# Kernel tuning notes

Hardware: AMD Instinct MI355X
Metric: run time of the kernel (lower is better)

Reference implementation:

```python
import jax, jax.numpy as jnp
import numpy as np

N, E, D, T = 10000, 320000, 128, 128


def _layer_norm(x, g, b, eps=1e-5):
    mu = jnp.mean(x, axis=-1, keepdims=True)
    var = jnp.mean(jnp.square(x - mu), axis=-1, keepdims=True)
    return (x - mu) * jax.lax.rsqrt(var + eps) * g + b


def setup_inputs() -> dict:
    key = jax.random.key(0)
    ks = jax.random.split(key, 24)
    s = 0.05

    def lin(k, fin, fout):
        k1, k2 = jax.random.split(k)
        return (jax.random.normal(k1, (fin, fout), jnp.float32) * s,
                jax.random.normal(k2, (fout,), jnp.float32) * s)

    W_tp, b_tp = lin(ks[5], T, D)
    W_sg, b_sg = lin(ks[6], D, D)
    W_dg, b_dg = lin(ks[7], D, D)
    W_eg, b_eg = lin(ks[8], D, D)
    W_su, b_su = lin(ks[9], D, D)
    W_du, b_du = lin(ks[10], D, D)
    return {
        'node_feats': jax.random.normal(ks[0], (N, D), jnp.float32),
        'edge_feats': jax.random.normal(ks[1], (E, D), jnp.float32),
        'time_feats': jax.random.normal(ks[2], (N, T), jnp.float32),
        'src': jax.random.randint(ks[3], (E,), 0, N),
        'dst': jax.random.randint(ks[4], (E,), 0, N),
        'W_tp': W_tp, 'b_tp': b_tp,
        'W_sg': W_sg, 'b_sg': b_sg,
        'W_dg': W_dg, 'b_dg': b_dg,
        'W_eg': W_eg, 'b_eg': b_eg,
        'W_su': W_su, 'b_su': b_su,
        'W_du': W_du, 'b_du': b_du,
        'ln_e_g': jnp.ones((D,), jnp.float32), 'ln_e_b': jnp.zeros((D,), jnp.float32),
        'ln_n_g': jnp.ones((D,), jnp.float32), 'ln_n_b': jnp.zeros((D,), jnp.float32),
    }


def reference(node_feats, edge_feats, time_feats, src, dst,
              W_tp, b_tp, W_sg, b_sg, W_dg, b_dg, W_eg, b_eg,
              W_su, b_su, W_du, b_du, ln_e_g, ln_e_b, ln_n_g, ln_n_b):
    n_nodes = node_feats.shape[0]
    # per-node gate projections (time proj folded into source gate)
    e_src = node_feats @ W_sg + b_sg + time_feats @ W_tp + b_tp   # [N, D]
    e_dst = node_feats @ W_dg + b_dg                              # [N, D]
    # edge gating: gather from both endpoints + edge feature projection
    m = e_src[src] + e_dst[dst] + edge_feats @ W_eg + b_eg        # [E, D]
    sigma = jax.nn.sigmoid(m)                                     # [E, D]
    # gated message passing: scatter-add over destination nodes
    Bh = node_feats @ W_du + b_du                                 # [N, D]
    sum_sigma_h = jax.ops.segment_sum(Bh[src] * sigma, dst, num_segments=n_nodes)
    sum_sigma = jax.ops.segment_sum(sigma, dst, num_segments=n_nodes)
    h = sum_sigma_h / (sum_sigma + 1e-6)                          # [N, D]
    x = node_feats @ W_su + b_su + h
    x = jax.nn.silu(_layer_norm(x, ln_n_g, ln_n_b))
    y = jax.nn.silu(_layer_norm(m, ln_e_g, ln_e_b))
    x = node_feats + x  # residual
    y = edge_feats + y
    return (x, y)
```

## Files before the change

kernel.cpp:

```cpp
#include <hip/hip_runtime.h>
#include <hip/hip_bf16.h>

#define N_NODES 10000
#define N_EDGES 320000
#define D 128
#define NBINS 10000

typedef float f32x4 __attribute__((ext_vector_type(4)));
typedef float f32x2 __attribute__((ext_vector_type(2)));
typedef short bf16x8 __attribute__((ext_vector_type(8)));
typedef short bf16x16 __attribute__((ext_vector_type(16)));

static __device__ inline short f2bf(float f) {
    union { __hip_bfloat16 h; short s; } u;
    u.h = __float2bfloat16(f);
    return u.s;
}

static __device__ inline float bf2f(short s) {
    union { float f; unsigned u; } x;
    x.u = ((unsigned)(unsigned short)s) << 16;
    return x.f;
}

static __device__ inline float fast_rcp(float x) { return __builtin_amdgcn_rcpf(x); }

__global__ void prep_hist(const float* __restrict__ W_sg, const float* __restrict__ W_tp,
                          const float* __restrict__ W_dg, const float* __restrict__ W_du,
                          const float* __restrict__ W_su, const float* __restrict__ W_eg,
                          short* __restrict__ Wsrc, short* __restrict__ Wdg,
                          short* __restrict__ Wdu, short* __restrict__ Wsu,
                          short* __restrict__ Weg,
                          const int* __restrict__ dst, int* __restrict__ cnt) {
    int bid = blockIdx.x;
    if (bid < 1250) {
        int i = bid * 256 + threadIdx.x;
        atomicAdd(&cnt[dst[i]], 1);
        return;
    }
    int idx = (bid - 1250) * 256 + threadIdx.x;
    const float* W0; const float* W1; short* out; int i2;
    if (idx < 32768)      { W0 = W_sg; W1 = W_tp; out = Wsrc; i2 = idx; }
    else if (idx < 49152) { W0 = W_dg; W1 = W_dg; out = Wdg;  i2 = idx - 32768; }
    else if (idx < 65536) { W0 = W_du; W1 = W_du; out = Wdu;  i2 = idx - 49152; }
    else if (idx < 81920) { W0 = W_su; W1 = W_su; out = Wsu;  i2 = idx - 65536; }
    else                  { W0 = W_eg; W1 = W_eg; out = Weg;  i2 = idx - 81920; }
    int b  = i2 & 7;
    int l  = (i2 >> 3) & 63;
    int jt = (i2 >> 9) & 7;
    int t  = i2 >> 12;
    int k = 32 * t + ((l >> 4) * 8) + b;
    int j = jt * 16 + (l & 15);
    float v = (k < 128) ? W0[k * 128 + j] : W1[(k - 128) * 128 + j];
    out[i2] = f2bf(v);
}

__launch_bounds__(1024)
__global__ void scan_kernel(const int* __restrict__ cnt, int* __restrict__ cursor) {
    __shared__ int s[1024];
    int t = threadIdx.x;
    int b0 = t * 10;
    int loc[10];
    int tot = 0;
#pragma unroll
    for (int i = 0; i < 10; ++i) {
        int v = (b0 + i < NBINS) ? cnt[b0 + i] : 0;
        loc[i] = tot; tot += v;
    }
    s[t] = tot;
    __syncthreads();
    for (int off = 1; off < 1024; off <<= 1) {
        int v = (t >= off) ? s[t - off] : 0;
        __syncthreads();
        s[t] += v;
        __syncthreads();
    }
    int base = (t == 0) ? 0 : s[t - 1];
#pragma unroll
    for (int i = 0; i < 10; ++i)
        if (b0 + i < NBINS) cursor[b0 + i] = base + loc[i];
}

__global__ void scatter_kernel(const int* __restrict__ src, const int* __restrict__ dst,
                               int* __restrict__ cursor,
                               int* __restrict__ perm,
                               int* __restrict__ src_s, int* __restrict__ dst_s) {
    int i = blockIdx.x * 256 + threadIdx.x;
    if (i < N_EDGES) {
        int d = dst[i];
        int p = atomicAdd(&cursor[d], 1);
        perm[p] = i;
        src_s[p] = src[i];
        dst_s[p] = d;
    }
}

__launch_bounds__(256)
__global__ void node_proj_kernel(const float* __restrict__ node,
                                 const float* __restrict__ timef,
                                 const short* __restrict__ Wsrc_pk,
                                 const short* __restrict__ Wdg_pk,
                                 const short* __restrict__ Wdu_pk,
                                 const short* __restrict__ Wsu_pk,
                                 const float* __restrict__ b_sg, const float* __restrict__ b_tp,
                                 const float* __restrict__ b_dg, const float* __restrict__ b_du,
                                 const float* __restrict__ b_su, const float* __restrict__ b_eg,
                                 short* __restrict__ spk,
                                 short* __restrict__ dpk,
                                 float* __restrict__ xs,
                                 float* __restrict__ ss, float* __restrict__ ssh) {
    {
        int r0b = blockIdx.x * 64;
        int nrows = N_NODES - r0b; if (nrows > 64) nrows = 64;
        f32x4 z = {0.f, 0.f, 0.f, 0.f};
        f32x4* s4 = (f32x4*)(ss + (size_t)r0b * D);
        f32x4* h4 = (f32x4*)(ssh + (size_t)r0b * D);
        int nch = nrows * D / 4;
        for (int i = threadIdx.x; i < nch; i += 256) { s4[i] = z; h4[i] = z; }
    }

    int tid = threadIdx.x;
    int w = tid >> 6;
    int l = tid & 63;
    int g = l >> 4;
    int lr = l & 15;
    int r0 = blockIdx.x * 64 + w * 16;
    int arow = r0 + lr;

    bf16x8 aN[4], aT[4];
    if (arow < N_NODES) {
        const float* np = node + (size_t)arow * D;
        const float* tp = timef + (size_t)arow * D;
#pragma unroll
        for (int t = 0; t < 4; ++t) {
            int k0 = 32 * t + g * 8;
            f32x4 v0 = *(const f32x4*)(np + k0);
            f32x4 v1 = *(const f32x4*)(np + k0 + 4);
            f32x4 u0 = *(const f32x4*)(tp + k0);
            f32x4 u1 = *(const f32x4*)(tp + k0 + 4);
            bf16x8 a, b;
#pragma unroll
            for (int i = 0; i < 4; ++i) {
                a[i] = f2bf(v0[i]); a[4 + i] = f2bf(v1[i]);
                b[i] = f2bf(u0[i]); b[4 + i] = f2bf(u1[i]);
            }
            aN[t] = a; aT[t] = b;
        }
    } else {
        bf16x8 z = {0, 0, 0, 0, 0, 0, 0, 0};
#pragma unroll
        for (int t = 0; t < 4; ++t) { aN[t] = z; aT[t] = z; }
    }

    const bf16x8* Bsrc = (const bf16x8*)Wsrc_pk;
    const bf16x8* Bdg  = (const bf16x8*)Wdg_pk;
    const bf16x8* Bdu  = (const bf16x8*)Wdu_pk;
    const bf16x8* Bsu  = (const bf16x8*)Wsu_pk;

    {
        bf16x8 chunk[4];
#pragma unroll
        for (int jt = 0; jt < 8; ++jt) {
            int c = jt * 16 + lr;
            f32x4 acc = {0.f, 0.f, 0.f, 0.f};
#pragma unroll
            for (int t = 0; t < 4; ++t)
                acc = __builtin_amdgcn_mfma_f32_16x16x32_bf16(aN[t], Bsrc[(t * 8 + jt) * 64 + l], acc, 0, 0, 0);
#pragma unroll
            for (int t = 0; t < 4; ++t)
                acc = __builtin_amdgcn_mfma_f32_16x16x32_bf16(aT[t], Bsrc[((4 + t) * 8 + jt) * 64 + l], acc, 0, 0, 0);
            float bias = b_sg[c] + b_tp[c];
#pragma unroll
            for (int r = 0; r < 4; ++r) chunk[r][jt] = f2bf(acc[r] + bias);
        }
#pragma unroll
        for (int r = 0; r < 4; ++r) {
            int row = r0 + g * 4 + r;
            if (row < N_NODES) *(bf16x8*)(spk + (size_t)row * 256 + lr * 16) = chunk[r];
        }
    }

    {
        bf16x8 chD[4], chH[4];
        float xsv[4][8];
#pragma unroll
        for (int jt = 0; jt < 8; ++jt) {
            int c = jt * 16 + lr;
            f32x4 a0 = {0.f, 0.f, 0.f, 0.f}, a1 = a0, a2 = a0;
#pragma unroll
            for (int t = 0; t < 4; ++t) {
                a0 = __builtin_amdgcn_mfma_f32_16x16x32_bf16(aN[t], Bdg[(t * 8 + jt) * 64 + l], a0, 0, 0, 0);
                a1 = __builtin_amdgcn_mfma_f32_16x16x32_bf16(aN[t], Bdu[(t * 8 + jt) * 64 + l], a1, 0, 0, 0);
                a2 = __builtin_amdgcn_mfma_f32_16x16x32_bf16(aN[t], Bsu[(t * 8 + jt) * 64 + l], a2, 0, 0, 0);
            }
            float bdgc = b_dg[c] + b_eg[c];
            float bdu = b_du[c], bsu = b_su[c];
#pragma unroll
            for (int r = 0; r < 4; ++r) {
                chD[r][jt] = f2bf(a0[r] + bdgc);
                chH[r][jt] = f2bf(a1[r] + bdu);
                xsv[r][jt] = a2[r] + bsu;
            }
        }
#pragma unroll
        for (int r = 0; r < 4; ++r) {
            int row = r0 + g * 4 + r;
            if (row < N_NODES) {
                *(bf16x8*)(dpk + (size_t)row * D + lr * 8) = chD[r];
                *(bf16x8*)(spk + (size_t)row * 256 + lr * 16 + 8) = chH[r];
#pragma unroll
                for (int jt = 0; jt < 8; ++jt)
                    xs[(size_t)row * D + jt * 16 + lr] = xsv[r][jt];
            }
        }
    }
}


#define TILE_LOAD_IDX(S, E0) \
    const int eA##S = perm[(E0) + lr]; \
    int eidx##S[4], sidx##S[4], didx##S[4]; \
    _Pragma("unroll") \
    for (int r = 0; r < 4; ++r) { \
        int p = (E0) + g * 4 + r; \
        eidx##S[r] = perm[p]; sidx##S[r] = src_s[p]; didx##S[r] = dst_s[p]; \
    } \
    const int df##S = __shfl(didx##S[0], 0); \
    const bool uni##S = (df##S == __shfl(didx##S[3], 48));

#define TILE_GATHER(S) \
    bf16x16 esbh##S[4]; bf16x8 edv##S[4]; \
    _Pragma("unroll") \
    for (int r = 0; r < 4; ++r) \
        esbh##S[r] = *(const bf16x16*)(spk + (size_t)sidx##S[r] * 256 + lr * 16); \
    edv##S[0] = *(const bf16x8*)(dpk + (size_t)didx##S[0] * D + lr * 8); \
    if (!uni##S) { \
        _Pragma("unroll") \
        for (int r = 1; r < 4; ++r) \
            edv##S[r] = *(const bf16x8*)(dpk + (size_t)didx##S[r] * D + lr * 8); \
    } else { edv##S[1] = edv##S[0]; edv##S[2] = edv##S[0]; edv##S[3] = edv##S[0]; }

#define TILE_AFRAG(S) \
    bf16x8 aE##S[4]; \
    { const float* ep = edgef + (size_t)eA##S * D; \
      _Pragma("unroll") \
      for (int t = 0; t < 4; ++t) { \
        int k0 = 32 * t + g * 8; \
        f32x4 v0 = *(const f32x4*)(ep + k0); \
        f32x4 v1 = *(const f32x4*)(ep + k0 + 4); \
        bf16x8 a; \
        _Pragma("unroll") \
        for (int i = 0; i < 4; ++i) { a[i] = f2bf(v0[i]); a[4 + i] = f2bf(v1[i]); } \
        aE##S[t] = a; } }

#define TILE_COMPUTE(S) \
    f32x4 acc##S[8]; \
    _Pragma("unroll") \
    for (int jt = 0; jt < 8; ++jt) { \
        f32x4 c4 = {0.f, 0.f, 0.f, 0.f}; \
        _Pragma("unroll") \
        for (int t = 0; t < 4; ++t) \
            c4 = __builtin_amdgcn_mfma_f32_16x16x32_bf16(aE##S[t], Bp[(t * 8 + jt) * 64 + l], c4, 0, 0, 0); \
        acc##S[jt] = c4; } \
    float sum##S[4] = {0.f, 0.f, 0.f, 0.f}, sq##S[4] = {0.f, 0.f, 0.f, 0.f}; \
    _Pragma("unroll") \
    for (int jt = 0; jt < 8; ++jt) { \
        int c = jt * 16 + lr; \
        float sg[4], bsg[4]; \
        _Pragma("unroll") \
        for (int r = 0; r < 4; ++r) { \
            float m = acc##S[jt][r] + bf2f(esbh##S[r][jt]) + bf2f(edv##S[r][jt]); \
            acc##S[jt][r] = m; \
            float s = fast_rcp(1.f + __expf(-m)); \
            sg[r] = s; bsg[r] = bf2f(esbh##S[r][8 + jt]) * s; \
            sum##S[r] += m; sq##S[r] += m * m; } \
        if (uni##S) { \
            float aS = (sg[0] + sg[1]) + (sg[2] + sg[3]); \
            float aH = (bsg[0] + bsg[1]) + (bsg[2] + bsg[3]); \
            aS += __shfl_xor(aS, 16); aH += __shfl_xor(aH, 16); \
            aS += __shfl_xor(aS, 32); aH += __shfl_xor(aH, 32); \
            if (g == 0) { \
                atomicAdd(&ss [(size_t)df##S * D + c], aS); \
                atomicAdd(&ssh[(size_t)df##S * D + c], aH); } \
        } else { \
            float aS = sg[0], aH = bsg[0]; \
            _Pragma("unroll") \
            for (int r = 1; r < 4; ++r) { \
                if (didx##S[r] == didx##S[r - 1]) { aS += sg[r]; aH += bsg[r]; } \
                else { \
                    atomicAdd(&ss [(size_t)didx##S[r - 1] * D + c], aS); \
                    atomicAdd(&ssh[(size_t)didx##S[r - 1] * D + c], aH); \
                    aS = sg[r]; aH = bsg[r]; } } \
            atomicAdd(&ss [(size_t)didx##S[3] * D + c], aS); \
            atomicAdd(&ssh[(size_t)didx##S[3] * D + c], aH); } }

#define TILE_EPILOGUE(S) \
    _Pragma("unroll") \
    for (int r = 0; r < 4; ++r) { \
        float s = sum##S[r], q = sq##S[r]; \
        _Pragma("unroll") \
        for (int mk = 1; mk < 16; mk <<= 1) { s += __shfl_xor(s, mk); q += __shfl_xor(q, mk); } \
        float mean = s * (1.f / D); \
        sum##S[r] = mean; \
        sq##S[r] = rsqrtf(q * (1.f / D) - mean * mean + 1e-5f); } \
    _Pragma("unroll") \
    for (int jt = 0; jt < 8; ++jt) { \
        int c = jt * 16 + lr; \
        float gc = ln_g[c], bc = ln_b[c]; \
        _Pragma("unroll") \
        for (int r = 0; r < 4; ++r) { \
            float v = (acc##S[jt][r] - sum##S[r]) * sq##S[r] * gc + bc; \
            float sl = v * fast_rcp(1.f + __expf(-v)); \
            size_t off = (size_t)eidx##S[r] * D + c; \
            y[off] = __builtin_nontemporal_load(&edgef[off]) + sl; } }

__launch_bounds__(256)
__global__ void edge_kernel(const float* __restrict__ edgef,
                            const int* __restrict__ perm,
                            const int* __restrict__ src_s, const int* __restrict__ dst_s,
                            const short* __restrict__ Weg_pk,
                            const short* __restrict__ spk,
                            const short* __restrict__ dpk,
                            const float* __restrict__ ln_g, const float* __restrict__ ln_b,
                            float* __restrict__ ss, float* __restrict__ ssh,
                            float* __restrict__ y) {
    __shared__ short Bs[128 * 128];
    {
        const bf16x8* gw = (const bf16x8*)Weg_pk;
        bf16x8* sw = (bf16x8*)Bs;
        for (int i = threadIdx.x; i < 2048; i += 256) sw[i] = gw[i];
    }
    __syncthreads();

    int tid = threadIdx.x;
    int w = tid >> 6;
    int l = tid & 63;
    int g = l >> 4;
    int lr = l & 15;

    int b = blockIdx.x;
    const int q = 312, rr = 4;
    int xcd = b & 7, boff = b >> 3;
    int swz = (xcd < rr ? xcd * (q + 1) : rr * (q + 1) + (xcd - rr) * q) + boff;
    int ebase = swz * 128 + w * 32;

    const bf16x8* Bp = (const bf16x8*)Bs;

    TILE_LOAD_IDX(0, ebase)
    TILE_LOAD_IDX(1, ebase + 16)
    TILE_GATHER(0)
    TILE_AFRAG(0)
    TILE_AFRAG(1)
    TILE_COMPUTE(0)
    TILE_GATHER(1)
    TILE_EPILOGUE(0)
    TILE_COMPUTE(1)
    TILE_EPILOGUE(1)
}

__launch_bounds__(256)
__global__ void node_out_kernel(const float* __restrict__ node,
                                const float* __restrict__ xs,
                                const float* __restrict__ ssh, const float* __restrict__ ss,
                                const float* __restrict__ ln_g, const float* __restrict__ ln_b,
                                float* __restrict__ x) {
    int w = threadIdx.x >> 6;
    int l = threadIdx.x & 63;
    int row = blockIdx.x * 4 + w;
    if (row >= N_NODES) return;
    size_t base = (size_t)row * D + 2 * l;
    f32x2 xv = *(const f32x2*)(xs + base);
    f32x2 hs = *(const f32x2*)(ssh + base);
    f32x2 sv = *(const f32x2*)(ss + base);
    float v0 = xv[0] + hs[0] / (sv[0] + 1e-6f);
    float v1 = xv[1] + hs[1] / (sv[1] + 1e-6f);
    float s = v0 + v1, q = v0 * v0 + v1 * v1;
#pragma unroll
    for (int mk = 1; mk < 64; mk <<= 1) { s += __shfl_xor(s, mk); q += __shfl_xor(q, mk); }
    float mean = s * (1.f / D);
    float var = q * (1.f / D) - mean * mean;
    float rstd = rsqrtf(var + 1e-5f);
    float t0 = (v0 - mean) * rstd * ln_g[2 * l] + ln_b[2 * l];
    float t1 = (v1 - mean) * rstd * ln_g[2 * l + 1] + ln_b[2 * l + 1];
    t0 = t0 * fast_rcp(1.f + __expf(-t0));
    t1 = t1 * fast_rcp(1.f + __expf(-t1));
    f32x2 nv = *(const f32x2*)(node + base);
    f32x2 outv;
    outv[0] = nv[0] + t0;
    outv[1] = nv[1] + t1;
    *(f32x2*)(x + base) = outv;
}

extern "C" void kernel_launch(void* const* d_in, const int* in_sizes, int n_in,
                              void* d_out, int out_size, void* d_ws, size_t ws_size,
                              hipStream_t stream) {
    const float* node  = (const float*)d_in[0];
    const float* edgef = (const float*)d_in[1];
    const float* timef = (const float*)d_in[2];
    const int*   src   = (const int*)d_in[3];
    const int*   dst   = (const int*)d_in[4];
    const float* W_tp = (const float*)d_in[5];  const float* b_tp = (const float*)d_in[6];
    const float* W_sg = (const float*)d_in[7];  const float* b_sg = (const float*)d_in[8];
    const float* W_dg = (const float*)d_in[9];  const float* b_dg = (const float*)d_in[10];
    const float* W_eg = (const float*)d_in[11]; const float* b_eg = (const float*)d_in[12];
    const float* W_su = (const float*)d_in[13]; const float* b_su = (const float*)d_in[14];
    const float* W_du = (const float*)d_in[15]; const float* b_du = (const float*)d_in[16];
    const float* ln_e_g = (const float*)d_in[17]; const float* ln_e_b = (const float*)d_in[18];
    const float* ln_n_g = (const float*)d_in[19]; const float* ln_n_b = (const float*)d_in[20];

    char* ws = (char*)d_ws;
    size_t nd = (size_t)N_NODES * D;
    float* ss    = (float*)ws; ws += nd * 4;
    float* ssh   = (float*)ws; ws += nd * 4;
    float* xs    = (float*)ws; ws += nd * 4;
    short* spk   = (short*)ws; ws += (size_t)N_NODES * 256 * 2;
    short* dpk   = (short*)ws; ws += nd * 2;
    short* Wsrc_pk = (short*)ws; ws += 256 * 128 * 2;
    short* Wdg_pk  = (short*)ws; ws += 128 * 128 * 2;
    short* Wdu_pk  = (short*)ws; ws += 128 * 128 * 2;
    short* Wsu_pk  = (short*)ws; ws += 128 * 128 * 2;
    short* Weg_pk  = (short*)ws; ws += 128 * 128 * 2;
    int* cnt       = (int*)ws; ws += 10240 * 4;
    int* cursor    = (int*)ws; ws += 10240 * 4;
    int* perm      = (int*)ws; ws += (size_t)N_EDGES * 4;
    int* src_s     = (int*)ws; ws += (size_t)N_EDGES * 4;
    int* dst_s     = (int*)ws; ws += (size_t)N_EDGES * 4;

    hipMemsetAsync(cnt, 0, 10240 * 4, stream);

    prep_hist<<<1634, 256, 0, stream>>>(W_sg, W_tp, W_dg, W_du, W_su, W_eg,
                                        Wsrc_pk, Wdg_pk, Wdu_pk, Wsu_pk, Weg_pk,
                                        dst, cnt);
    scan_kernel<<<1, 1024, 0, stream>>>(cnt, cursor);
    scatter_kernel<<<(N_EDGES + 255) / 256, 256, 0, stream>>>(src, dst, cursor, perm, src_s, dst_s);

    node_proj_kernel<<<(N_NODES + 63) / 64, 256, 0, stream>>>(
        node, timef, Wsrc_pk, Wdg_pk, Wdu_pk, Wsu_pk,
        b_sg, b_tp, b_dg, b_du, b_su, b_eg, spk, dpk, xs, ss, ssh);

    edge_kernel<<<2500, 256, 0, stream>>>(
        edgef, perm, src_s, dst_s, Weg_pk, spk, dpk,
        ln_e_g, ln_e_b, ss, ssh, (float*)d_out + nd);

    node_out_kernel<<<N_NODES / 4, 256, 0, stream>>>(
        node, xs, ssh, ss, ln_n_g, ln_n_b, (float*)d_out);
}
```

Measured before the change: 256.4 us.

## Persist edge kernel over chunks, combine tile atomics, shuffle-load indices, memset accumulators

The edge kernel becomes a persistent grid of 1256 blocks that loops over 2500 chunks. When both 16-edge tiles of a wave go to the same destination node, their atomics are merged into one, which halves atomic traffic for those cases. Index loads become one coalesced load per lane, spread by shuffles. Zeroing of the ss/ssh accumulators moves from node_proj_kernel into a single memset, and the nontemporal load of edge features in the epilogue becomes a plain load. The occupancy hint is raised to 4 blocks per CU, which may limit registers and cause spills.

```diff
diff --git a/kernel.cpp b/kernel.cpp
--- a/kernel.cpp
+++ b/kernel.cpp
@@ -5,6 +5,8 @@
 #define N_EDGES 320000
 #define D 128
 #define NBINS 10000
+#define NCHUNKS 2500
+#define EDGE_GRID 1256
 
 typedef float f32x4 __attribute__((ext_vector_type(4)));
 typedef float f32x2 __attribute__((ext_vector_type(2)));
@@ -107,18 +109,7 @@
                                  const float* __restrict__ b_su, const float* __restrict__ b_eg,
                                  short* __restrict__ spk,
                                  short* __restrict__ dpk,
-                                 float* __restrict__ xs,
-                                 float* __restrict__ ss, float* __restrict__ ssh) {
-    {
-        int r0b = blockIdx.x * 64;
-        int nrows = N_NODES - r0b; if (nrows > 64) nrows = 64;
-        f32x4 z = {0.f, 0.f, 0.f, 0.f};
-        f32x4* s4 = (f32x4*)(ss + (size_t)r0b * D);
-        f32x4* h4 = (f32x4*)(ssh + (size_t)r0b * D);
-        int nch = nrows * D / 4;
-        for (int i = threadIdx.x; i < nch; i += 256) { s4[i] = z; h4[i] = z; }
-    }
-
+                                 float* __restrict__ xs) {
     int tid = threadIdx.x;
     int w = tid >> 6;
     int l = tid & 63;
@@ -218,15 +209,19 @@
 
 
 #define TILE_LOAD_IDX(S, E0) \
-    const int eA##S = perm[(E0) + lr]; \
+    const int pm##S = perm[(E0) + lr]; \
+    const int sv##S = src_s[(E0) + lr]; \
+    const int dv##S = dst_s[(E0) + lr]; \
     int eidx##S[4], sidx##S[4], didx##S[4]; \
     _Pragma("unroll") \
     for (int r = 0; r < 4; ++r) { \
-        int p = (E0) + g * 4 + r; \
-        eidx##S[r] = perm[p]; sidx##S[r] = src_s[p]; didx##S[r] = dst_s[p]; \
+        int qq = g * 4 + r; \
+        eidx##S[r] = __shfl(pm##S, qq); \
+        sidx##S[r] = __shfl(sv##S, qq); \
+        didx##S[r] = __shfl(dv##S, qq); \
     } \
-    const int df##S = __shfl(didx##S[0], 0); \
-    const bool uni##S = (df##S == __shfl(didx##S[3], 48));
+    const int df##S = __shfl(dv##S, 0); \
+    const bool uni##S = (df##S == __shfl(dv##S, 15));
 
 #define TILE_GATHER(S) \
     bf16x16 esbh##S[4]; bf16x8 edv##S[4]; \
@@ -242,7 +237,7 @@
 
 #define TILE_AFRAG(S) \
     bf16x8 aE##S[4]; \
-    { const float* ep = edgef + (size_t)eA##S * D; \
+    { const float* ep = edgef + (size_t)pm##S * D; \
       _Pragma("unroll") \
       for (int t = 0; t < 4; ++t) { \
         int k0 = 32 * t + g * 8; \
@@ -253,7 +248,7 @@
         for (int i = 0; i < 4; ++i) { a[i] = f2bf(v0[i]); a[4 + i] = f2bf(v1[i]); } \
         aE##S[t] = a; } }
 
-#define TILE_COMPUTE(S) \
+#define TILE_COMPUTE(S, DEFER, ADDPREV) \
     f32x4 acc##S[8]; \
     _Pragma("unroll") \
     for (int jt = 0; jt < 8; ++jt) { \
@@ -279,9 +274,12 @@
             float aH = (bsg[0] + bsg[1]) + (bsg[2] + bsg[3]); \
             aS += __shfl_xor(aS, 16); aH += __shfl_xor(aH, 16); \
             aS += __shfl_xor(aS, 32); aH += __shfl_xor(aH, 32); \
-            if (g == 0) { \
-                atomicAdd(&ss [(size_t)df##S * D + c], aS); \
-                atomicAdd(&ssh[(size_t)df##S * D + c], aH); } \
+            if (DEFER && comb) { aS0[jt] = aS; aH0[jt] = aH; } \
+            else { \
+                if (ADDPREV && comb) { aS += aS0[jt]; aH += aH0[jt]; } \
+                if (g == 0) { \
+                    atomicAdd(&ss [(size_t)df##S * D + c], aS); \
+                    atomicAdd(&ssh[(size_t)df##S * D + c], aH); } } \
         } else { \
             float aS = sg[0], aH = bsg[0]; \
             _Pragma("unroll") \
@@ -312,9 +310,9 @@
             float v = (acc##S[jt][r] - sum##S[r]) * sq##S[r] * gc + bc; \
             float sl = v * fast_rcp(1.f + __expf(-v)); \
             size_t off = (size_t)eidx##S[r] * D + c; \
-            y[off] = __builtin_nontemporal_load(&edgef[off]) + sl; } }
-
-__launch_bounds__(256)
+            y[off] = edgef[off] + sl; } }
+
+__launch_bounds__(256, 4)
 __global__ void edge_kernel(const float* __restrict__ edgef,
                             const int* __restrict__ perm,
                             const int* __restrict__ src_s, const int* __restrict__ dst_s,
@@ -337,25 +335,27 @@
     int l = tid & 63;
     int g = l >> 4;
     int lr = l & 15;
-
-    int b = blockIdx.x;
-    const int q = 312, rr = 4;
-    int xcd = b & 7, boff = b >> 3;
-    int swz = (xcd < rr ? xcd * (q + 1) : rr * (q + 1) + (xcd - rr) * q) + boff;
-    int ebase = swz * 128 + w * 32;
-
     const bf16x8* Bp = (const bf16x8*)Bs;
 
-    TILE_LOAD_IDX(0, ebase)
-    TILE_LOAD_IDX(1, ebase + 16)
-    TILE_GATHER(0)
-    TILE_AFRAG(0)
-    TILE_AFRAG(1)
-    TILE_COMPUTE(0)
-    TILE_GATHER(1)
-    TILE_EPILOGUE(0)
-    TILE_COMPUTE(1)
-    TILE_EPILOGUE(1)
+    for (int cc = blockIdx.x; cc < NCHUNKS; cc += EDGE_GRID) {
+        int xcd = cc & 7, boff = cc >> 3;
+        int swz = (xcd < 4 ? xcd * 313 : 1252 + (xcd - 4) * 312) + boff;
+        int ebase = swz * 128 + w * 32;
+
+        TILE_LOAD_IDX(0, ebase)
+        TILE_LOAD_IDX(1, ebase + 16)
+        const bool comb = uni0 && uni1 && (df0 == df1);
+        float aS0[8], aH0[8];
+
+        TILE_GATHER(0)
+        TILE_AFRAG(0)
+        TILE_AFRAG(1)
+        TILE_COMPUTE(0, 1, 0)
+        TILE_GATHER(1)
+        TILE_EPILOGUE(0)
+        TILE_COMPUTE(1, 0, 1)
+        TILE_EPILOGUE(1)
+    }
 }
 
 __launch_bounds__(256)
@@ -410,6 +410,8 @@
 
     char* ws = (char*)d_ws;
     size_t nd = (size_t)N_NODES * D;
+    int* cnt       = (int*)ws; ws += 10240 * 4;
+    int* cursor    = (int*)ws; ws += 10240 * 4;
     float* ss    = (float*)ws; ws += nd * 4;
     float* ssh   = (float*)ws; ws += nd * 4;
     float* xs    = (float*)ws; ws += nd * 4;
@@ -420,13 +422,11 @@
     short* Wdu_pk  = (short*)ws; ws += 128 * 128 * 2;
     short* Wsu_pk  = (short*)ws; ws += 128 * 128 * 2;
     short* Weg_pk  = (short*)ws; ws += 128 * 128 * 2;
-    int* cnt       = (int*)ws; ws += 10240 * 4;
-    int* cursor    = (int*)ws; ws += 10240 * 4;
     int* perm      = (int*)ws; ws += (size_t)N_EDGES * 4;
     int* src_s     = (int*)ws; ws += (size_t)N_EDGES * 4;
     int* dst_s     = (int*)ws; ws += (size_t)N_EDGES * 4;
 
-    hipMemsetAsync(cnt, 0, 10240 * 4, stream);
+    hipMemsetAsync(cnt, 0, 2 * 10240 * 4 + 2 * nd * 4, stream);
 
     prep_hist<<<1634, 256, 0, stream>>>(W_sg, W_tp, W_dg, W_du, W_su, W_eg,
                                         Wsrc_pk, Wdg_pk, Wdu_pk, Wsu_pk, Weg_pk,
@@ -436,9 +436,9 @@
 
     node_proj_kernel<<<(N_NODES + 63) / 64, 256, 0, stream>>>(
         node, timef, Wsrc_pk, Wdg_pk, Wdu_pk, Wsu_pk,
-        b_sg, b_tp, b_dg, b_du, b_su, b_eg, spk, dpk, xs, ss, ssh);
-
-    edge_kernel<<<2500, 256, 0, stream>>>(
+        b_sg, b_tp, b_dg, b_du, b_su, b_eg, spk, dpk, xs);
+
+    edge_kernel<<<EDGE_GRID, 256, 0, stream>>>(
         edgef, perm, src_s, dst_s, Weg_pk, spk, dpk,
         ln_e_g, ln_e_b, ss, ssh, (float*)d_out + nd);
 
```

Result: slower. 581.2 us (+126.7%).
